# Kernel optimization log

Hardware: AMD Instinct MI355X
Metric: run time of the kernel (lower is better)

The kernel has to match this reference:

```python
import jax, jax.numpy as jnp
import numpy as np

T, IN, H, OUT, L = 2048, 128, 128, 128, 2


def setup_inputs() -> dict:
    key = jax.random.key(0)
    ks = jax.random.split(key, 12)
    s_in = 1.0 / np.sqrt(IN)
    s_h = 1.0 / np.sqrt(H)
    s_ff = 1.0 / np.sqrt(2 * H)
    return {
        "emb": jax.random.normal(ks[0], (T, IN), jnp.float32),
        "start": jax.random.randint(ks[1], (T,), 0, 2).astype(jnp.int32),
        "w_in": jax.random.normal(ks[2], (H, IN), jnp.float32) * s_in,
        "b_in": jnp.zeros((H,), jnp.float32),
        "w_out": jax.random.normal(ks[3], (OUT, H), jnp.float32) * s_h,
        "b_out": jnp.zeros((OUT,), jnp.float32),
        "w_f": jax.random.normal(ks[4], (L, 1, H), jnp.float32) * s_h,
        "b_f": jnp.zeros((L, 1), jnp.float32),
        "w_i": jax.random.normal(ks[5], (L, 1, H), jnp.float32) * s_h,
        "b_i": jnp.zeros((L, 1), jnp.float32),
        "w_v": jax.random.normal(ks[6], (L, H, H), jnp.float32) * s_h,
        "b_v": jnp.zeros((L, H), jnp.float32),
        "w_q": jax.random.normal(ks[7], (L, H, H), jnp.float32) * s_h,
        "b_q": jnp.zeros((L, H), jnp.float32),
        "w_k": jax.random.normal(ks[8], (L, H, H), jnp.float32) * s_h,
        "b_k": jnp.zeros((L, H), jnp.float32),
        "w_o": jax.random.normal(ks[9], (L, H, H), jnp.float32) * s_h,
        "b_o": jnp.zeros((L, H), jnp.float32),
        "w_ff": jax.random.normal(ks[10], (L, H, 2 * H), jnp.float32) * s_ff,
        "b_ff": jnp.zeros((L, H), jnp.float32),
    }


def _mlstm_layer(x, gate_mask, w_f, b_f, w_i, b_i, w_v, b_v, w_q, b_q, w_k, b_k, w_o, b_o):
    # x: [T, H] layer input; gate_mask: [T] (0.0 at episode starts -> reset)
    Hdim = x.shape[-1]
    i = jnp.exp(x @ w_i.T + b_i)                           # [T, 1] exp input gate
    v = x @ w_v.T + b_v                                    # [T, H]
    k = (x * (1.0 / np.sqrt(Hdim))) @ w_k.T + b_k          # [T, H] (1/sqrt(H) applied before Linear)
    C = i[:, :, None] * (v[:, :, None] * k[:, None, :])    # [T, H, H] gated outer products
    n = i * k                                              # [T, H]
    g = jax.nn.sigmoid(x @ w_f.T + b_f)[:, 0] * gate_mask  # [T] forget gate, zeroed at resets

    def step(carry, inp):
        S, m = carry
        Ct, nt, gt = inp
        S = gt * S + Ct
        m = gt * m + nt
        return (S, m), (S, m)

    init = (jnp.zeros((Hdim, Hdim), x.dtype), jnp.zeros((Hdim,), x.dtype))
    _, (S_all, m_all) = jax.lax.scan(step, init, (C, n, g))  # [T,H,H], [T,H]

    q = x @ w_q.T + b_q                                    # [T, H]
    o = jax.nn.sigmoid(x @ w_o.T + b_o)                    # [T, H]
    num = jnp.einsum('thk,tk->th', S_all, q)               # C @ q per step
    den = jnp.maximum(jnp.abs(jnp.einsum('th,th->t', m_all, q))[:, None], 1.0)
    return o * (num / den)


def reference(emb, start, w_in, b_in, w_out, b_out, w_f, b_f, w_i, b_i,
              w_v, b_v, w_q, b_q, w_k, b_k, w_o, b_o, w_ff, b_ff):
    gate_mask = 1.0 - start.astype(emb.dtype)              # reset => discard previous state
    e = emb @ w_in.T + b_in                                # [T, H]
    z = e
    for l in range(w_f.shape[0]):
        h = _mlstm_layer(z, gate_mask, w_f[l], b_f[l], w_i[l], b_i[l],
                         w_v[l], b_v[l], w_q[l], b_q[l], w_k[l], b_k[l], w_o[l], b_o[l])
        z = jax.nn.leaky_relu(jnp.concatenate([h, e], axis=-1) @ w_ff[l].T + b_ff[l])
    return z @ w_out.T + b_out
```

## Files before the change

kernel.cpp:

```cpp
#include <hip/hip_runtime.h>
#include <math.h>

#define TT 2048
#define HH 128
#define ROWS 8
#define SP 132
#define XR 144
#define NBLK (TT / ROWS)

__device__ __forceinline__ float dot4(float4 a, float4 b) {
    return a.x * b.x + a.y * b.y + a.z * b.z + a.w * b.w;
}

__device__ __forceinline__ int xidx(int r, int k) {
    return r * XR + ((k >> 5) * 36) + (k & 31);
}

__device__ __forceinline__ float2 load_f2_agent(const float* p) {
    unsigned long long u = __hip_atomic_load((const unsigned long long*)p,
                                             __ATOMIC_RELAXED, __HIP_MEMORY_SCOPE_AGENT);
    float2 r;
    r.x = __uint_as_float((unsigned)(u & 0xffffffffull));
    r.y = __uint_as_float((unsigned)(u >> 32));
    return r;
}
__device__ __forceinline__ float load_f_agent(const float* p) {
    return __hip_atomic_load(p, __ATOMIC_RELAXED, __HIP_MEMORY_SCOPE_AGENT);
}
__device__ __forceinline__ void store_f_agent(float* p, float v) {
    __hip_atomic_store(p, v, __ATOMIC_RELAXED, __HIP_MEMORY_SCOPE_AGENT);
}
__device__ __forceinline__ unsigned load_u_agent(const unsigned* p) {
    return __hip_atomic_load(p, __ATOMIC_RELAXED, __HIP_MEMORY_SCOPE_AGENT);
}

__global__ __launch_bounds__(256) void prep_kernel(
        const float* __restrict__ w_in, const float* __restrict__ w_out,
        const float* __restrict__ w_v, const float* __restrict__ w_q,
        const float* __restrict__ w_k, const float* __restrict__ w_o,
        const float* __restrict__ w_ff, const int* __restrict__ start,
        float4* __restrict__ win_p, float4* __restrict__ wout_p,
        float4* __restrict__ wcat, float4* __restrict__ wff_p,
        int* __restrict__ stb, unsigned* __restrict__ flags) {
    if (blockIdx.x >= 224) {
        __shared__ int sl[256];
        int base = (blockIdx.x - 224) * 256;
        int t = base + threadIdx.x;
        sl[threadIdx.x] = start[t];
        __syncthreads();
        int s = t;
        while (s > base && sl[s - base] == 0) --s;
        if (s == base && sl[0] == 0) {
            while (s > 0 && start[s] == 0) --s;
        }
        stb[t] = s;
        return;
    }
    if (blockIdx.x == 0) flags[threadIdx.x] = 0u;
    int i = blockIdx.x * 256 + threadIdx.x;
    if (i < 4096) {
        int cg = i >> 7, col = i & 127;
        win_p[i] = ((const float4*)w_in)[col * 32 + cg];
    } else if (i < 8192) {
        int j = i - 4096, cg = j >> 7, col = j & 127;
        wout_p[j] = ((const float4*)w_out)[col * 32 + cg];
    } else if (i < 40960) {
        int j = i - 8192;
        int l = j >> 14, r = j & 16383, cg = r >> 9, col = r & 511;
        int sel = col >> 7, cm = col & 127;
        const float* s = (sel == 0 ? w_v : sel == 1 ? w_q : sel == 2 ? w_k : w_o) + l * HH * HH;
        wcat[j] = ((const float4*)s)[cm * 32 + cg];
    } else {
        int j = i - 40960;
        int l = j >> 13, r = j & 8191, cg = r >> 7, col = r & 127;
        const float* s = w_ff + l * HH * 256;
        wff_p[j] = ((const float4*)s)[col * 64 + cg];
    }
}

__device__ __forceinline__ void attn_row(int t0, int bid, unsigned phase,
        const unsigned* __restrict__ flags,
        const float* __restrict__ kb, const float* __restrict__ vb,
        const float* __restrict__ kl, const float* __restrict__ vl,
        const float* __restrict__ qs, const float* __restrict__ os,
        const float* __restrict__ g, const float* __restrict__ iexp,
        const float* __restrict__ gl, const float* __restrict__ il,
        const int* __restrict__ stb, float* __restrict__ hs) {
    int tid = threadIdx.x;
    int wv = tid >> 6, lane = tid & 63;
    int t = t0 + wv;
    int st = stb[t];
    float2 q2 = *(const float2*)(qs + wv * SP + 2 * lane);
    float2 o2 = *(const float2*)(os + wv * SP + 2 * lane);
    float nx = 0.f, ny = 0.f, dsum = 0.f, decay = 1.f;
    int lo = st > t0 ? st : t0;
    for (int tp = t; tp >= lo; --tp) {
        int r = tp - t0;
        float2 k2 = *(const float2*)(kl + r * SP + 2 * lane);
        float2 v2 = *(const float2*)(vl + r * SP + 2 * lane);
        float p = k2.x * q2.x + k2.y * q2.y;
#pragma unroll
        for (int off = 1; off <= 32; off <<= 1) p += __shfl_xor(p, off, 64);
        float coeff = decay * il[r] * p;
        nx += coeff * v2.x; ny += coeff * v2.y; dsum += coeff;
        if (tp > st) decay *= gl[r];
    }
    if (st < t0) {
        for (int j = st >> 3; j < bid; ++j) {
            while (load_u_agent(flags + j) < phase) __builtin_amdgcn_s_sleep(1);
        }
        int tp = t0 - 1;
        while (tp >= st) {
            int nb = tp - st + 1; if (nb > 4) nb = 4;
            float2 kk[4], vv[4];
            float ie[4], gv[4];
#pragma unroll
            for (int b = 0; b < 4; ++b) {
                if (b < nb) {
                    kk[b] = load_f2_agent(kb + (tp - b) * HH + 2 * lane);
                    vv[b] = load_f2_agent(vb + (tp - b) * HH + 2 * lane);
                    ie[b] = load_f_agent(iexp + (tp - b));
                    gv[b] = load_f_agent(g + (tp - b));
                }
            }
#pragma unroll
            for (int b = 0; b < 4; ++b) {
                if (b < nb) {
                    float p = kk[b].x * q2.x + kk[b].y * q2.y;
#pragma unroll
                    for (int off = 1; off <= 32; off <<= 1) p += __shfl_xor(p, off, 64);
                    float coeff = decay * ie[b] * p;
                    nx += coeff * vv[b].x; ny += coeff * vv[b].y; dsum += coeff;
                    if (tp - b > st) decay *= gv[b];
                }
            }
            tp -= nb;
        }
    }
    float inv = 1.f / fmaxf(fabsf(dsum), 1.f);
    int d = 2 * lane;
    *(float2*)(hs + wv * XR + (d >> 5) * 36 + (d & 31)) =
        make_float2(o2.x * nx * inv, o2.y * ny * inv);
}

__device__ __forceinline__ void proj_fi(int t0, const float* __restrict__ xls,
        const float* __restrict__ w_f, const float* __restrict__ b_f,
        const float* __restrict__ w_i, const float* __restrict__ b_i,
        const int* __restrict__ start, float* __restrict__ g, float* __restrict__ iexp,
        float* __restrict__ gl, float* __restrict__ il) {
    int tid = threadIdx.x;
    int wv = tid >> 6, lane = tid & 63;
    if (wv >= 8) return;
    int d = 2 * lane;
    float2 xv = *(const float2*)(xls + wv * XR + (d >> 5) * 36 + (d & 31));
    float pf = xv.x * w_f[d] + xv.y * w_f[d + 1];
    float pi = xv.x * w_i[d] + xv.y * w_i[d + 1];
#pragma unroll
    for (int off = 1; off <= 32; off <<= 1) {
        pf += __shfl_xor(pf, off, 64);
        pi += __shfl_xor(pi, off, 64);
    }
    if (lane == 0) {
        int t = t0 + wv;
        float gvv = start[t] ? 0.f : 1.f / (1.f + expf(-(pf + b_f[0])));
        float ivv = expf(pi + b_i[0]);
        store_f_agent(g + t, gvv);
        store_f_agent(iexp + t, ivv);
        gl[wv] = gvv;
        il[wv] = ivv;
    }
}

__device__ __forceinline__ void proj_block(int t0, const float* __restrict__ xls,
        const float4* __restrict__ wc,
        const float* __restrict__ b_v, const float* __restrict__ b_q,
        const float* __restrict__ b_k, const float* __restrict__ b_o,
        float* __restrict__ kb, float* __restrict__ vb,
        float* __restrict__ kl, float* __restrict__ vl,
        float* __restrict__ qs, float* __restrict__ os) {
    int tid = threadIdx.x;
    int lane = tid & 63, w = tid >> 6;
    int kc = lane >> 4, c = lane & 15;
    int cslot = (w & 7) * 16 + c;
    int mp = w >> 3;
    float a0[8] = {}, a1[8] = {};
#pragma unroll
    for (int j = 0; j < 8; ++j) {
        const float4* wb = wc + (kc * 8 + j) * 512 + mp * 256;
        float4 w0 = wb[cslot];
        float4 w1 = wb[128 + cslot];
#pragma unroll
        for (int rr = 0; rr < 8; ++rr) {
            float4 x4 = *(const float4*)(xls + rr * XR + kc * 36 + 4 * j);
            a0[rr] += dot4(x4, w0);
            a1[rr] += dot4(x4, w1);
        }
    }
#pragma unroll
    for (int rr = 0; rr < 8; ++rr) {
        a0[rr] += __shfl_xor(a0[rr], 16, 64); a0[rr] += __shfl_xor(a0[rr], 32, 64);
        a1[rr] += __shfl_xor(a1[rr], 16, 64); a1[rr] += __shfl_xor(a1[rr], 32, 64);
    }
    if (kc == 0) {
        if (mp == 0) {
            float bv = b_v[cslot], bq = b_q[cslot];
#pragma unroll
            for (int rr = 0; rr < 8; ++rr) {
                float vv = a0[rr] + bv;
                store_f_agent(vb + (t0 + rr) * HH + cslot, vv);
                vl[rr * SP + cslot] = vv;
                qs[rr * SP + cslot] = a1[rr] + bq;
            }
        } else {
            const float ks = 0.088388347648318447f;
            float bk = b_k[cslot], bo = b_o[cslot];
#pragma unroll
            for (int rr = 0; rr < 8; ++rr) {
                float kk = a0[rr] * ks + bk;
                store_f_agent(kb + (t0 + rr) * HH + cslot, kk);
                kl[rr * SP + cslot] = kk;
                os[rr * SP + cslot] = 1.f / (1.f + expf(-(a1[rr] + bo)));
            }
        }
    }
}

__device__ __forceinline__ void ffe_block(const float* __restrict__ esb,
        const float4* __restrict__ wffg, float* __restrict__ zp) {
    int tid = threadIdx.x;
    int lane = tid & 63, w = tid >> 6;
    int kc = lane >> 4, c = lane & 15;
    int cslot = (w - 8) * 16 + c;
    float acc[8] = {};
#pragma unroll
    for (int j = 0; j < 8; ++j) {
        float4 w0 = wffg[(32 + kc * 8 + j) * 128 + cslot];
#pragma unroll
        for (int rr = 0; rr < 8; ++rr) {
            float4 x4 = *(const float4*)(esb + rr * XR + kc * 36 + 4 * j);
            acc[rr] += dot4(x4, w0);
        }
    }
#pragma unroll
    for (int rr = 0; rr < 8; ++rr) {
        acc[rr] += __shfl_xor(acc[rr], 16, 64);
        acc[rr] += __shfl_xor(acc[rr], 32, 64);
    }
    if (kc == 0) {
#pragma unroll
        for (int rr = 0; rr < 8; ++rr) zp[rr * SP + cslot] = acc[rr];
    }
}

__device__ __forceinline__ void ffh_block(const float* __restrict__ hsb,
        const float4* wshl, const float* __restrict__ zp,
        const float* __restrict__ b_ff, float* __restrict__ zs) {
    int tid = threadIdx.x;
    int lane = tid & 63, w = tid >> 6;
    int kc = lane >> 4, c = lane & 15;
    int rg = w >> 3;
    int cslot = (w & 7) * 16 + c;
    float acc[4] = {};
#pragma unroll
    for (int j = 0; j < 8; ++j) {
        float4 w0 = wshl[(kc * 8 + j) * 128 + cslot];
#pragma unroll
        for (int rr = 0; rr < 4; ++rr) {
            float4 x4 = *(const float4*)(hsb + (rg * 4 + rr) * XR + kc * 36 + 4 * j);
            acc[rr] += dot4(x4, w0);
        }
    }
#pragma unroll
    for (int rr = 0; rr < 4; ++rr) {
        acc[rr] += __shfl_xor(acc[rr], 16, 64);
        acc[rr] += __shfl_xor(acc[rr], 32, 64);
    }
    if (kc == 0) {
        float bb = b_ff[cslot];
#pragma unroll
        for (int rr = 0; rr < 4; ++rr) {
            int r = rg * 4 + rr;
            float z = acc[rr] + zp[r * SP + cslot] + bb;
            z = z > 0.f ? z : 0.01f * z;
            zs[xidx(r, cslot)] = z;
        }
    }
}

__device__ __forceinline__ void dense128(int t0, const float* __restrict__ xls,
        const float4* __restrict__ Wp, const float* __restrict__ b,
        float* __restrict__ yg, float* __restrict__ ys) {
    int tid = threadIdx.x;
    int lane = tid & 63, w = tid >> 6;
    int kc = lane >> 3, c = lane & 7;
    int col = (w >> 3) * 64 + (w & 7) * 8 + c;
    float a0[8] = {};
#pragma unroll
    for (int j = 0; j < 4; ++j) {
        float4 w0 = Wp[(kc * 4 + j) * 128 + col];
        int off = (kc >> 1) * 36 + (kc & 1) * 16 + 4 * j;
#pragma unroll
        for (int rr = 0; rr < 8; ++rr) {
            float4 x4 = *(const float4*)(xls + rr * XR + off);
            a0[rr] += dot4(x4, w0);
        }
    }
#pragma unroll
    for (int rr = 0; rr < 8; ++rr) {
        a0[rr] += __shfl_xor(a0[rr], 8, 64);
        a0[rr] += __shfl_xor(a0[rr], 16, 64);
        a0[rr] += __shfl_xor(a0[rr], 32, 64);
    }
    if (kc == 0) {
        float bb = b[col];
#pragma unroll
        for (int rr = 0; rr < 8; ++rr) {
            float y = a0[rr] + bb;
            if (ys) ys[xidx(rr, col)] = y;
            if (yg) yg[(t0 + rr) * HH + col] = y;
        }
    }
}

__device__ __forceinline__ void stage_wsh_h(const float4* __restrict__ src, float4* lds) {
    int tid2 = threadIdx.x - 512;
    int wv2 = tid2 >> 6;
#pragma unroll
    for (int it = 0; it < 8; ++it) {
        __builtin_amdgcn_global_load_lds(
            (const __attribute__((address_space(1))) unsigned int*)(src + it * 512 + tid2),
            (__attribute__((address_space(3))) unsigned int*)(lds + it * 512 + wv2 * 64),
            16, 0, 0);
    }
}

__global__ __launch_bounds__(1024, 4) void mega_kernel(
        const float* __restrict__ emb, const int* __restrict__ start,
        const float4* __restrict__ win_p, const float* __restrict__ b_in,
        const float4* __restrict__ wcat,
        const float* __restrict__ b_v, const float* __restrict__ b_q,
        const float* __restrict__ b_k, const float* __restrict__ b_o,
        const float* __restrict__ w_f, const float* __restrict__ b_f,
        const float* __restrict__ w_i, const float* __restrict__ b_i,
        const float4* __restrict__ wff_p, const float* __restrict__ b_ff,
        const float4* __restrict__ wout_p, const float* __restrict__ b_out,
        float* __restrict__ k0b, float* __restrict__ v0b,
        float* __restrict__ k1b, float* __restrict__ v1b,
        float* __restrict__ g0, float* __restrict__ i0,
        float* __restrict__ g1, float* __restrict__ i1,
        const int* __restrict__ stb, unsigned* __restrict__ flags,
        float* __restrict__ out) {
    __shared__ float xs[ROWS * XR];
    __shared__ float es[ROWS * XR];
    __shared__ float hs[ROWS * XR];
    __shared__ float zs[ROWS * XR];
    __shared__ float qs[ROWS * SP];
    __shared__ float os[ROWS * SP];
    __shared__ float zp[ROWS * SP];
    __shared__ float kl[ROWS * SP];
    __shared__ float vl[ROWS * SP];
    __shared__ float gl[ROWS], il[ROWS];
    __shared__ float4 wsh[4096];
    int tid = threadIdx.x;
    int bid = blockIdx.x;
    int t0 = bid * ROWS;
    int wv = tid >> 6;

    {
        int row = tid >> 7, dd = tid & 127;
        xs[row * XR + (dd >> 5) * 36 + (dd & 31)] = emb[(t0 + row) * HH + dd];
    }
    __syncthreads();
    dense128(t0, xs, win_p, b_in, (float*)0, es);
    __syncthreads();
    proj_block(t0, es, wcat, b_v, b_q, b_k, b_o, k0b, v0b, kl, vl, qs, os);
    proj_fi(t0, es, w_f, b_f, w_i, b_i, start, g0, i0, gl, il);
    __syncthreads();
    if (tid == 0)
        __hip_atomic_store(flags + bid, 1u, __ATOMIC_RELAXED, __HIP_MEMORY_SCOPE_AGENT);

    if (wv < 8) {
        attn_row(t0, bid, 1u, flags, k0b, v0b, kl, vl, qs, os, g0, i0, gl, il, stb, hs);
    } else {
        stage_wsh_h(wff_p, wsh);
        ffe_block(es, wff_p, zp);
    }
    __syncthreads();
    ffh_block(hs, wsh, zp, b_ff, zs);
    __syncthreads();
    proj_block(t0, zs, wcat + 16384, b_v + HH, b_q + HH, b_k + HH, b_o + HH,
               k1b, v1b, kl, vl, qs, os);
    proj_fi(t0, zs, w_f + HH, b_f + 1, w_i + HH, b_i + 1, start, g1, i1, gl, il);
    __syncthreads();
    if (tid == 0)
        __hip_atomic_store(flags + bid, 2u, __ATOMIC_RELAXED, __HIP_MEMORY_SCOPE_AGENT);

    if (wv < 8) {
        attn_row(t0, bid, 2u, flags, k1b, v1b, kl, vl, qs, os, g1, i1, gl, il, stb, hs);
    } else {
        stage_wsh_h(wff_p + 8192, wsh);
        ffe_block(es, wff_p + 8192, zp);
    }
    __syncthreads();
    ffh_block(hs, wsh, zp, b_ff + HH, zs);
    __syncthreads();
    dense128(t0, zs, wout_p, b_out, out, (float*)0);
}

extern "C" void kernel_launch(void* const* d_in, const int* in_sizes, int n_in,
                              void* d_out, int out_size, void* d_ws, size_t ws_size,
                              hipStream_t stream) {
    const float* emb   = (const float*)d_in[0];
    const int*   start = (const int*)  d_in[1];
    const float* w_in  = (const float*)d_in[2];
    const float* b_in  = (const float*)d_in[3];
    const float* w_out = (const float*)d_in[4];
    const float* b_out = (const float*)d_in[5];
    const float* w_f   = (const float*)d_in[6];
    const float* b_f   = (const float*)d_in[7];
    const float* w_i   = (const float*)d_in[8];
    const float* b_i   = (const float*)d_in[9];
    const float* w_v   = (const float*)d_in[10];
    const float* b_v   = (const float*)d_in[11];
    const float* w_q   = (const float*)d_in[12];
    const float* b_q   = (const float*)d_in[13];
    const float* w_k   = (const float*)d_in[14];
    const float* b_k   = (const float*)d_in[15];
    const float* w_o   = (const float*)d_in[16];
    const float* b_o   = (const float*)d_in[17];
    const float* w_ff  = (const float*)d_in[18];
    const float* b_ff  = (const float*)d_in[19];
    float* out = (float*)d_out;

    unsigned* flags = (unsigned*)d_ws;
    float* ws = (float*)d_ws + 256;
    float* k0b = ws; ws += TT * HH;
    float* v0b = ws; ws += TT * HH;
    float* k1b = ws; ws += TT * HH;
    float* v1b = ws; ws += TT * HH;
    float* g0  = ws; ws += TT;
    float* i0  = ws; ws += TT;
    float* g1  = ws; ws += TT;
    float* i1  = ws; ws += TT;
    int* stb   = (int*)ws; ws += TT;
    float4* win_p  = (float4*)ws; ws += 16384;
    float4* wout_p = (float4*)ws; ws += 16384;
    float4* wcat   = (float4*)ws; ws += 131072;
    float4* wff_p  = (float4*)ws; ws += 65536;

    prep_kernel<<<dim3(232), dim3(256), 0, stream>>>(
        w_in, w_out, w_v, w_q, w_k, w_o, w_ff, start,
        win_p, wout_p, wcat, wff_p, stb, flags);
    mega_kernel<<<dim3(NBLK), dim3(1024), 0, stream>>>(
        emb, start, win_p, b_in, wcat,
        b_v, b_q, b_k, b_o, w_f, b_f, w_i, b_i,
        wff_p, b_ff, wout_p, b_out,
        k0b, v0b, k1b, v1b, g0, i0, g1, i1,
        stb, flags, out);
}
```

Measured before the change: 125.2 us.

## Batch in-block attention loads and split projection work by rows

The in-block attention loop now loads up to eight k/v rows and their gate values from LDS into registers before doing the reductions, which removes the serial load-then-reduce dependency on each step. The projection block now gives each wave group four rows across all four projections instead of eight rows across two projections. That changes how weights and inputs are reused and leaves every lane holding four accumulator arrays. The fixed unroll of eight assumes that ROWS equals 8, and the projection change raises register pressure while cutting the number of x loads per weight.

Result: no change. 125.9 us (+0.5%).

```diff
diff --git a/kernel.cpp b/kernel.cpp
--- a/kernel.cpp
+++ b/kernel.cpp
@@ -94,16 +94,29 @@
     float2 o2 = *(const float2*)(os + wv * SP + 2 * lane);
     float nx = 0.f, ny = 0.f, dsum = 0.f, decay = 1.f;
     int lo = st > t0 ? st : t0;
-    for (int tp = t; tp >= lo; --tp) {
-        int r = tp - t0;
-        float2 k2 = *(const float2*)(kl + r * SP + 2 * lane);
-        float2 v2 = *(const float2*)(vl + r * SP + 2 * lane);
-        float p = k2.x * q2.x + k2.y * q2.y;
-#pragma unroll
-        for (int off = 1; off <= 32; off <<= 1) p += __shfl_xor(p, off, 64);
-        float coeff = decay * il[r] * p;
-        nx += coeff * v2.x; ny += coeff * v2.y; dsum += coeff;
-        if (tp > st) decay *= gl[r];
+    int n = t - lo + 1;
+    float2 kk8[8], vv8[8];
+    float ie8[8], gv8[8];
+#pragma unroll
+    for (int b = 0; b < 8; ++b) {
+        if (b < n) {
+            int r = (t - b) - t0;
+            kk8[b] = *(const float2*)(kl + r * SP + 2 * lane);
+            vv8[b] = *(const float2*)(vl + r * SP + 2 * lane);
+            ie8[b] = il[r];
+            gv8[b] = gl[r];
+        }
+    }
+#pragma unroll
+    for (int b = 0; b < 8; ++b) {
+        if (b < n) {
+            float p = kk8[b].x * q2.x + kk8[b].y * q2.y;
+#pragma unroll
+            for (int off = 1; off <= 32; off <<= 1) p += __shfl_xor(p, off, 64);
+            float coeff = decay * ie8[b] * p;
+            nx += coeff * vv8[b].x; ny += coeff * vv8[b].y; dsum += coeff;
+            if (t - b > st) decay *= gv8[b];
+        }
     }
     if (st < t0) {
         for (int j = st >> 3; j < bid; ++j) {
@@ -182,45 +195,45 @@
     int lane = tid & 63, w = tid >> 6;
     int kc = lane >> 4, c = lane & 15;
     int cslot = (w & 7) * 16 + c;
-    int mp = w >> 3;
-    float a0[8] = {}, a1[8] = {};
+    int r0 = (w >> 3) * 4;
+    float av[4] = {}, aq[4] = {}, ak[4] = {}, ao[4] = {};
 #pragma unroll
     for (int j = 0; j < 8; ++j) {
-        const float4* wb = wc + (kc * 8 + j) * 512 + mp * 256;
+        const float4* wb = wc + (kc * 8 + j) * 512;
         float4 w0 = wb[cslot];
         float4 w1 = wb[128 + cslot];
-#pragma unroll
-        for (int rr = 0; rr < 8; ++rr) {
-            float4 x4 = *(const float4*)(xls + rr * XR + kc * 36 + 4 * j);
-            a0[rr] += dot4(x4, w0);
-            a1[rr] += dot4(x4, w1);
-        }
-    }
-#pragma unroll
-    for (int rr = 0; rr < 8; ++rr) {
-        a0[rr] += __shfl_xor(a0[rr], 16, 64); a0[rr] += __shfl_xor(a0[rr], 32, 64);
-        a1[rr] += __shfl_xor(a1[rr], 16, 64); a1[rr] += __shfl_xor(a1[rr], 32, 64);
+        float4 w2 = wb[256 + cslot];
+        float4 w3 = wb[384 + cslot];
+#pragma unroll
+        for (int rr = 0; rr < 4; ++rr) {
+            float4 x4 = *(const float4*)(xls + (r0 + rr) * XR + kc * 36 + 4 * j);
+            av[rr] += dot4(x4, w0);
+            aq[rr] += dot4(x4, w1);
+            ak[rr] += dot4(x4, w2);
+            ao[rr] += dot4(x4, w3);
+        }
+    }
+#pragma unroll
+    for (int rr = 0; rr < 4; ++rr) {
+        av[rr] += __shfl_xor(av[rr], 16, 64); av[rr] += __shfl_xor(av[rr], 32, 64);
+        aq[rr] += __shfl_xor(aq[rr], 16, 64); aq[rr] += __shfl_xor(aq[rr], 32, 64);
+        ak[rr] += __shfl_xor(ak[rr], 16, 64); ak[rr] += __shfl_xor(ak[rr], 32, 64);
+        ao[rr] += __shfl_xor(ao[rr], 16, 64); ao[rr] += __shfl_xor(ao[rr], 32, 64);
     }
     if (kc == 0) {
-        if (mp == 0) {
-            float bv = b_v[cslot], bq = b_q[cslot];
-#pragma unroll
-            for (int rr = 0; rr < 8; ++rr) {
-                float vv = a0[rr] + bv;
-                store_f_agent(vb + (t0 + rr) * HH + cslot, vv);
-                vl[rr * SP + cslot] = vv;
-                qs[rr * SP + cslot] = a1[rr] + bq;
-            }
-        } else {
-            const float ks = 0.088388347648318447f;
-            float bk = b_k[cslot], bo = b_o[cslot];
-#pragma unroll
-            for (int rr = 0; rr < 8; ++rr) {
-                float kk = a0[rr] * ks + bk;
-                store_f_agent(kb + (t0 + rr) * HH + cslot, kk);
-                kl[rr * SP + cslot] = kk;
-                os[rr * SP + cslot] = 1.f / (1.f + expf(-(a1[rr] + bo)));
-            }
+        const float ks = 0.088388347648318447f;
+        float bv = b_v[cslot], bq = b_q[cslot], bk = b_k[cslot], bo = b_o[cslot];
+#pragma unroll
+        for (int rr = 0; rr < 4; ++rr) {
+            int r = r0 + rr, t = t0 + r;
+            float vvv = av[rr] + bv;
+            float kkk = ak[rr] * ks + bk;
+            store_f_agent(vb + t * HH + cslot, vvv);
+            vl[r * SP + cslot] = vvv;
+            store_f_agent(kb + t * HH + cslot, kkk);
+            kl[r * SP + cslot] = kkk;
+            qs[r * SP + cslot] = aq[rr] + bq;
+            os[r * SP + cslot] = 1.f / (1.f + expf(-(ao[rr] + bo)));
         }
     }
 }
```
